# Kernel optimization log

Measured on AMD Instinct MI355X. Metric: run time of the kernel, lower is better.

## Reference

```python
import jax, jax.numpy as jnp
import numpy as np

N = 50000      # nodes
E = 800000     # edges
F_IN = 128     # in_channels
C = 64         # hidden_channels (per-head out channels)
H = 2          # heads
G = 256        # num graphs in batch
NEG_SLOPE = 0.2


def _gat_conv(x, src, dst, e_attr, W, att_src, att_dst, We, att_e, bias):
    """PyG GATConv with edge_dim, heads=H, concat=False, add_self_loops=True.
    x: [N, Fin]; src/dst: [Etot] (self-loops already appended); e_attr: [Etot, 1]."""
    n = x.shape[0]
    xp = (x @ W).reshape(n, H, C)                       # [N,H,C]
    ep = (e_attr @ We).reshape(-1, H, C)                # [Etot,H,C]
    a_src = jnp.einsum('nhc,hc->nh', xp, att_src)       # [N,H]
    a_dst = jnp.einsum('nhc,hc->nh', xp, att_dst)
    a_e = jnp.einsum('ehc,hc->eh', ep, att_e)
    alpha = a_src[src] + a_dst[dst] + a_e               # [Etot,H]
    alpha = jax.nn.leaky_relu(alpha, NEG_SLOPE)
    # softmax over edges grouped by destination node
    amax = jax.ops.segment_max(alpha, dst, num_segments=n)
    ex = jnp.exp(alpha - amax[dst])
    denom = jax.ops.segment_sum(ex, dst, num_segments=n)
    coef = ex / denom[dst]                              # [Etot,H]
    msg = coef[:, :, None] * xp[src]                    # [Etot,H,C]
    out = jax.ops.segment_sum(msg, dst, num_segments=n)  # [N,H,C]
    return out.mean(axis=1) + bias                      # concat=False -> head mean


def _add_self_loops(edge_index, edge_attr, n):
    loop = jnp.arange(n, dtype=edge_index.dtype)
    src = jnp.concatenate([edge_index[0], loop])
    dst = jnp.concatenate([edge_index[1], loop])
    fill = jnp.broadcast_to(edge_attr.mean(axis=0, keepdims=True), (n, edge_attr.shape[1]))
    ea = jnp.concatenate([edge_attr, fill], axis=0)
    return src, dst, ea


def setup_inputs() -> dict:
    key = jax.random.key(0)
    ks = jax.random.split(key, 20)
    s = 0.1
    inp = {
        'x': jax.random.normal(ks[0], (N, F_IN), jnp.float32),
        'edge_index': jax.random.randint(ks[1], (2, E), 0, N, jnp.int64),
        'edge_attr': jax.random.normal(ks[2], (E, 1), jnp.float32),
        'batch': jnp.sort(jax.random.randint(ks[3], (N,), 0, G, jnp.int64)),
        # GAT layer 1
        'W1': jax.random.normal(ks[4], (F_IN, H * C), jnp.float32) * s,
        'att_src1': jax.random.normal(ks[5], (H, C), jnp.float32) * s,
        'att_dst1': jax.random.normal(ks[6], (H, C), jnp.float32) * s,
        'We1': jax.random.normal(ks[7], (1, H * C), jnp.float32) * s,
        'att_e1': jax.random.normal(ks[8], (H, C), jnp.float32) * s,
        'b1': jnp.zeros((C,), jnp.float32),
        # GAT layer 2
        'W2': jax.random.normal(ks[9], (C, H * C), jnp.float32) * s,
        'att_src2': jax.random.normal(ks[10], (H, C), jnp.float32) * s,
        'att_dst2': jax.random.normal(ks[11], (H, C), jnp.float32) * s,
        'We2': jax.random.normal(ks[12], (1, H * C), jnp.float32) * s,
        'att_e2': jax.random.normal(ks[13], (H, C), jnp.float32) * s,
        'b2': jnp.zeros((C,), jnp.float32),
        # final linear
        'lin_w': jax.random.normal(ks[14], (C, 1), jnp.float32) * s,
        'lin_b': jnp.zeros((1,), jnp.float32),
    }
    return inp


def reference(x, edge_index, edge_attr, batch, W1, att_src1, att_dst1, We1, att_e1, b1,
              W2, att_src2, att_dst2, We2, att_e2, b2, lin_w, lin_b):
    src, dst, ea = _add_self_loops(edge_index, edge_attr, x.shape[0])
    h = jax.nn.relu(_gat_conv(x, src, dst, ea, W1, att_src1, att_dst1, We1, att_e1, b1))
    h = jax.nn.relu(_gat_conv(h, src, dst, ea, W2, att_src2, att_dst2, We2, att_e2, b2))
    # global mean pool over graphs
    sums = jax.ops.segment_sum(h, batch, num_segments=G)            # [G,C]
    cnts = jax.ops.segment_sum(jnp.ones((x.shape[0],), h.dtype), batch, num_segments=G)
    pooled = sums / jnp.maximum(cnts, 1.0)[:, None]
    return (pooled @ lin_w + lin_b).squeeze(-1)                      # [G]
```

## Files before the change

kernel.cpp:

```cpp
#include <hip/hip_runtime.h>


#define NEG_SLOPE 0.2f
#define CAP 64
#define RNG 128
#define AEDGE 4096
#define BCAP 40
typedef unsigned int uint;

__device__ __forceinline__ float wred_sum(float v) {
#pragma unroll
  for (int m = 32; m; m >>= 1) v += __shfl_xor(v, m);
  return v;
}
__device__ __forceinline__ float wred_max(float v) {
#pragma unroll
  for (int m = 32; m; m >>= 1) v = fmaxf(v, __shfl_xor(v, m));
  return v;
}
__device__ __forceinline__ float lrelu(float x) {
  return x > 0.0f ? x : NEG_SLOPE * x;
}
__device__ __forceinline__ uint bfpack(float a, float b) {
  uint ua = __float_as_uint(a), ub = __float_as_uint(b);
  ua = (ua + 0x7FFFu + ((ua >> 16) & 1u)) >> 16;
  ub = (ub + 0x7FFFu + ((ub >> 16) & 1u)) >> 16;
  return ua | (ub << 16);
}
__device__ __forceinline__ float4 bfunpack(uint2 v) {
  float4 f;
  f.x = __uint_as_float(v.x << 16);
  f.y = __uint_as_float(v.x & 0xFFFF0000u);
  f.z = __uint_as_float(v.y << 16);
  f.w = __uint_as_float(v.y & 0xFFFF0000u);
  return f;
}

#define BM 64
#define BK 32
__global__ __launch_bounds__(256) void fused_bin_gemm(
    const int* __restrict__ ei, const float* __restrict__ eattr, int E,
    int nbins, int ablks, int2* __restrict__ buck, int* __restrict__ cnt,
    float* __restrict__ partials,
    const float* __restrict__ X, const float* __restrict__ W,
    const float* __restrict__ att_src, const float* __restrict__ att_dst,
    uint* __restrict__ Y16, float* __restrict__ a_src,
    float* __restrict__ a_dst, int Nn, int K) {
  __shared__ float As[BK][68];
  __shared__ float Bs[BK][64];
  int t = threadIdx.x;

  if ((int)blockIdx.x < ablks) {
    int blk = blockIdx.x;
    int* cursor = (int*)As;
    float* red = ((float*)As) + 512;
    for (int i = t; i < nbins; i += 256) cursor[i] = 0;
    __syncthreads();
    int base = blk * AEDGE + t;
    float easum = 0.f;
#pragma unroll
    for (int k = 0; k < AEDGE / 256; ++k) {
      int i = base + k * 256;
      if (i < E) {
        int dv = ei[E + i];
        int sv = ei[i];
        float ev = eattr[i];
        easum += ev;
        int b = dv >> 7;
        int slot = atomicAdd(&cursor[b], 1);
        if (slot < BCAP) {
          int2 pl;
          pl.x = (sv << 7) | (dv & 127);
          pl.y = __float_as_int(ev);
          buck[((size_t)blk * nbins + b) * BCAP + slot] = pl;
        }
      }
    }
    __syncthreads();
    for (int b = t; b < nbins; b += 256)
      cnt[(size_t)b * ablks + blk] = min(cursor[b], BCAP);
    __syncthreads();
    red[t] = easum;
    __syncthreads();
    for (int off = 128; off; off >>= 1) {
      if (t < off) red[t] += red[t + off];
      __syncthreads();
    }
    if (t == 0) partials[blk] = red[0];
    return;
  }

  int g = (int)blockIdx.x - ablks;
  int tx = t & 15;
  int ty = t >> 4;
  int half = g & 1;
  int rowBase = (g >> 1) * BM;
  float acc[4][4];
#pragma unroll
  for (int r = 0; r < 4; ++r)
#pragma unroll
    for (int c = 0; c < 4; ++c) acc[r][c] = 0.f;

  for (int k0 = 0; k0 < K; k0 += BK) {
#pragma unroll
    for (int v = t; v < 512; v += 256) {
      int r = v >> 3;
      int cv = v & 7;
      int gr = rowBase + r;
      float4 a = make_float4(0.f, 0.f, 0.f, 0.f);
      if (gr < Nn) a = *(const float4*)(X + (size_t)gr * K + k0 + cv * 4);
      As[cv * 4 + 0][r] = a.x;
      As[cv * 4 + 1][r] = a.y;
      As[cv * 4 + 2][r] = a.z;
      As[cv * 4 + 3][r] = a.w;
    }
#pragma unroll
    for (int v = t; v < 512; v += 256) {
      int r = v >> 4;
      int cv = v & 15;
      *(float4*)&Bs[r][cv * 4] =
          *(const float4*)(W + (size_t)(k0 + r) * 128 + half * 64 + cv * 4);
    }
    __syncthreads();
#pragma unroll
    for (int kk = 0; kk < BK; ++kk) {
      float4 a = *(const float4*)&As[kk][ty * 4];
      float4 b = *(const float4*)&Bs[kk][tx * 4];
      acc[0][0] = fmaf(a.x, b.x, acc[0][0]);
      acc[0][1] = fmaf(a.x, b.y, acc[0][1]);
      acc[0][2] = fmaf(a.x, b.z, acc[0][2]);
      acc[0][3] = fmaf(a.x, b.w, acc[0][3]);
      acc[1][0] = fmaf(a.y, b.x, acc[1][0]);
      acc[1][1] = fmaf(a.y, b.y, acc[1][1]);
      acc[1][2] = fmaf(a.y, b.z, acc[1][2]);
      acc[1][3] = fmaf(a.y, b.w, acc[1][3]);
      acc[2][0] = fmaf(a.z, b.x, acc[2][0]);
      acc[2][1] = fmaf(a.z, b.y, acc[2][1]);
      acc[2][2] = fmaf(a.z, b.z, acc[2][2]);
      acc[2][3] = fmaf(a.z, b.w, acc[2][3]);
      acc[3][0] = fmaf(a.w, b.x, acc[3][0]);
      acc[3][1] = fmaf(a.w, b.y, acc[3][1]);
      acc[3][2] = fmaf(a.w, b.z, acc[3][2]);
      acc[3][3] = fmaf(a.w, b.w, acc[3][3]);
    }
    __syncthreads();
  }

  float attS[4], attD[4];
#pragma unroll
  for (int c = 0; c < 4; ++c) {
    attS[c] = att_src[half * 64 + tx * 4 + c];
    attD[c] = att_dst[half * 64 + tx * 4 + c];
  }
#pragma unroll
  for (int r = 0; r < 4; ++r) {
    int gr = rowBase + ty * 4 + r;
    float ps = 0.f, pd = 0.f;
#pragma unroll
    for (int c = 0; c < 4; ++c) {
      ps = fmaf(acc[r][c], attS[c], ps);
      pd = fmaf(acc[r][c], attD[c], pd);
    }
#pragma unroll
    for (int m = 1; m < 16; m <<= 1) {
      ps += __shfl_xor(ps, m);
      pd += __shfl_xor(pd, m);
    }
    if (gr < Nn) {
      if (tx == 0) {
        a_src[gr * 2 + half] = ps;
        a_dst[gr * 2 + half] = pd;
      }
      uint2 pk;
      pk.x = bfpack(acc[r][0], acc[r][1]);
      pk.y = bfpack(acc[r][2], acc[r][3]);
      *(uint2*)(Y16 + (size_t)gr * 64 + half * 32 + tx * 2) = pk;
    }
  }
}

__global__ __launch_bounds__(256) void passB(const int2* __restrict__ buck,
                                             const int* __restrict__ cnt,
                                             int nbins, int ablks, int N,
                                             int2* __restrict__ pay,
                                             int* __restrict__ fills) {
  __shared__ int pre[256];
  __shared__ int hist[128];
  int b = blockIdx.x;
  int t = threadIdx.x;
  if (t < 128) hist[t] = 0;
  int c = (t < ablks) ? cnt[(size_t)b * ablks + t] : 0;
  pre[t] = c;
  __syncthreads();
  for (int off = 1; off < 256; off <<= 1) {
    int v = (t >= off) ? pre[t - off] : 0;
    __syncthreads();
    pre[t] += v;
    __syncthreads();
  }
  int T = pre[255];
  int nodeBase = b << 7;
  for (int idx = t; idx < T; idx += 256) {
    int lo = 0, hi = 255;
    while (lo < hi) {
      int mid = (lo + hi) >> 1;
      if (pre[mid] > idx)
        hi = mid;
      else
        lo = mid + 1;
    }
    int blk = lo;
    int within = idx - (blk ? pre[blk - 1] : 0);
    int2 pl = buck[((size_t)blk * nbins + b) * BCAP + within];
    int dlo = pl.x & 127;
    int sv = pl.x >> 7;
    int slot = atomicAdd(&hist[dlo], 1);
    if (slot < CAP - 1) {
      int2 o;
      o.x = sv;
      o.y = pl.y;
      pay[((size_t)(nodeBase + dlo) << 6) + slot] = o;
    }
  }
  __syncthreads();
  if (t < 128) {
    int n = nodeBase + t;
    if (n < N) fills[n] = min(hist[t], CAP - 1);
  }
}

__global__ void finalize_params(const float* __restrict__ partials, int nparts,
                                int E, const float* __restrict__ We1,
                                const float* __restrict__ atte1,
                                const float* __restrict__ We2,
                                const float* __restrict__ atte2,
                                const float* __restrict__ W2,
                                const float* __restrict__ atts2,
                                const float* __restrict__ attd2,
                                float* __restrict__ params,
                                float* __restrict__ avec) {
  __shared__ float sm[256];
  int t = threadIdx.x;
  float s = 0.f;
  for (int i = t; i < nparts; i += 256) s += partials[i];
  sm[t] = s;
  __syncthreads();
  for (int off = 128; off; off >>= 1) {
    if (t < off) sm[t] += sm[t + off];
    __syncthreads();
  }
  if (t == 0) params[0] = sm[0] / (float)E;
  __syncthreads();
  int l = t >> 7, h = (t >> 6) & 1, c = t & 63;
  float p = (l == 0) ? We1[h * 64 + c] * atte1[h * 64 + c]
                     : We2[h * 64 + c] * atte2[h * 64 + c];
  sm[t] = p;
  __syncthreads();
  for (int off = 32; off; off >>= 1) {
    if (c < off) sm[t] += sm[t + off];
    __syncthreads();
  }
  if (c == 0) params[1 + l * 2 + h] = sm[t];
  int k = t & 63;
  const float* att = (l == 0) ? atts2 : attd2;
  float acc = 0.f;
#pragma unroll 4
  for (int cc = 0; cc < 64; ++cc)
    acc = fmaf(W2[k * 128 + h * 64 + cc], att[h * 64 + cc], acc);
  avec[l * 128 + h * 64 + k] = acc;
}

__global__ __launch_bounds__(256, 8) void gat_gather_l1(
    const int* __restrict__ fills, const int2* __restrict__ pay,
    const uint* __restrict__ xp16, const float* __restrict__ a_src1,
    const float* __restrict__ a_dst, const float* __restrict__ params,
    const float* __restrict__ bias, const float* __restrict__ avec,
    uint* __restrict__ h16, float* __restrict__ a_src2,
    float* __restrict__ a_dst2, int N) {
  __shared__ float sm_c[4][128];
  __shared__ uint sm_s[4][64];
  int wid = threadIdx.x >> 6, lane = threadIdx.x & 63;
  int n = blockIdx.x * 4 + wid;
  if (n >= N) return;
  int beg = n << 6;
  int dg = min(fills[n], CAP - 1) + 1;
  float s0 = params[1], s1 = params[2];
  float ad0 = a_dst[n * 2 + 0], ad1 = a_dst[n * 2 + 1];
  const uint2* xp2 = (const uint2*)xp16;

  float al0 = -1e30f, al1 = -1e30f;
  uint myS = (uint)n * 32u;
  if (lane < dg) {
    int sidx = n;
    float eav = params[0];
    if (lane != dg - 1) {
      int2 pe = pay[beg + lane];
      sidx = pe.x;
      eav = __int_as_float(pe.y);
      myS = (uint)pe.x * 32u;
    }
    float2 as = *(const float2*)(a_src1 + (size_t)sidx * 2);
    al0 = lrelu(as.x + ad0 + eav * s0);
    al1 = lrelu(as.y + ad1 + eav * s1);
  }
  float m0 = wred_max(al0), m1 = wred_max(al1);
  float e0 = __expf(al0 - m0), e1 = __expf(al1 - m1);
  float sum0 = wred_sum(e0), sum1 = wred_sum(e1);
  sm_c[wid][lane * 2 + 0] = e0 / sum0;
  sm_c[wid][lane * 2 + 1] = e1 / sum1;
  sm_s[wid][lane] = myS;

  int half = lane >> 5;
  uint l5 = lane & 31;
  int h = (lane >> 4) & 1;
  const float* sc = sm_c[wid];
  const uint* ss = sm_s[wid];
  float4 acc = make_float4(0.f, 0.f, 0.f, 0.f);

  for (int e0i = 0; e0i < dg; e0i += 8) {
    int ea = e0i + half;
    int eb = e0i + 2 + half;
    int ec = e0i + 4 + half;
    int ed = e0i + 6 + half;
    uint2 ua = xp2[ss[ea] + l5];
    uint2 ub = xp2[ss[eb] + l5];
    uint2 uc = xp2[ss[ec] + l5];
    uint2 ud = xp2[ss[ed] + l5];
    float ca = sc[ea * 2 + h], cb = sc[eb * 2 + h];
    float cc2 = sc[ec * 2 + h], cd = sc[ed * 2 + h];
    float4 va = bfunpack(ua);
    float4 vb = bfunpack(ub);
    float4 vc = bfunpack(uc);
    float4 vd = bfunpack(ud);
    acc.x = fmaf(ca, va.x, acc.x);
    acc.y = fmaf(ca, va.y, acc.y);
    acc.z = fmaf(ca, va.z, acc.z);
    acc.w = fmaf(ca, va.w, acc.w);
    acc.x = fmaf(cb, vb.x, acc.x);
    acc.y = fmaf(cb, vb.y, acc.y);
    acc.z = fmaf(cb, vb.z, acc.z);
    acc.w = fmaf(cb, vb.w, acc.w);
    acc.x = fmaf(cc2, vc.x, acc.x);
    acc.y = fmaf(cc2, vc.y, acc.y);
    acc.z = fmaf(cc2, vc.z, acc.z);
    acc.w = fmaf(cc2, vc.w, acc.w);
    acc.x = fmaf(cd, vd.x, acc.x);
    acc.y = fmaf(cd, vd.y, acc.y);
    acc.z = fmaf(cd, vd.z, acc.z);
    acc.w = fmaf(cd, vd.w, acc.w);
  }

  acc.x += __shfl_xor(acc.x, 32);
  acc.y += __shfl_xor(acc.y, 32);
  acc.z += __shfl_xor(acc.z, 32);
  acc.w += __shfl_xor(acc.w, 32);
  float4 oth;
  oth.x = __shfl_xor(acc.x, 16);
  oth.y = __shfl_xor(acc.y, 16);
  oth.z = __shfl_xor(acc.z, 16);
  oth.w = __shfl_xor(acc.w, 16);

  float ps0 = 0.f, ps1 = 0.f, pd0 = 0.f, pd1 = 0.f;
  if (lane < 16) {
    float4 b = *(const float4*)(bias + lane * 4);
    float4 o;
    o.x = fmaxf(0.5f * (acc.x + oth.x) + b.x, 0.f);
    o.y = fmaxf(0.5f * (acc.y + oth.y) + b.y, 0.f);
    o.z = fmaxf(0.5f * (acc.z + oth.z) + b.z, 0.f);
    o.w = fmaxf(0.5f * (acc.w + oth.w) + b.w, 0.f);
    uint2 hp;
    hp.x = bfpack(o.x, o.y);
    hp.y = bfpack(o.z, o.w);
    *(uint2*)(h16 + (size_t)n * 32 + lane * 2) = hp;
    float4 vs0 = *(const float4*)(avec + lane * 4);
    float4 vs1 = *(const float4*)(avec + 64 + lane * 4);
    float4 vd0 = *(const float4*)(avec + 128 + lane * 4);
    float4 vd1 = *(const float4*)(avec + 192 + lane * 4);
    ps0 = o.x * vs0.x + o.y * vs0.y + o.z * vs0.z + o.w * vs0.w;
    ps1 = o.x * vs1.x + o.y * vs1.y + o.z * vs1.z + o.w * vs1.w;
    pd0 = o.x * vd0.x + o.y * vd0.y + o.z * vd0.z + o.w * vd0.w;
    pd1 = o.x * vd1.x + o.y * vd1.y + o.z * vd1.z + o.w * vd1.w;
  }
#pragma unroll
  for (int m = 1; m < 16; m <<= 1) {
    ps0 += __shfl_xor(ps0, m);
    ps1 += __shfl_xor(ps1, m);
    pd0 += __shfl_xor(pd0, m);
    pd1 += __shfl_xor(pd1, m);
  }
  if (lane == 0) {
    a_src2[n * 2 + 0] = ps0;
    a_src2[n * 2 + 1] = ps1;
    a_dst2[n * 2 + 0] = pd0;
    a_dst2[n * 2 + 1] = pd1;
  }
}

__global__ __launch_bounds__(256, 8) void gat_gather_l2(
    const int* __restrict__ fills, const int2* __restrict__ pay,
    const uint* __restrict__ h16, const float* __restrict__ a_src,
    const float* __restrict__ a_dst, const float* __restrict__ params,
    float* __restrict__ agg, int N) {
  __shared__ float sm_c[4][128];
  __shared__ uint sm_s[4][64];
  int wid = threadIdx.x >> 6, lane = threadIdx.x & 63;
  int n = blockIdx.x * 4 + wid;
  if (n >= N) return;
  int beg = n << 6;
  int dg = min(fills[n], CAP - 1) + 1;
  float s0 = params[3], s1 = params[4];
  float ad0 = a_dst[n * 2 + 0], ad1 = a_dst[n * 2 + 1];
  const uint2* h2 = (const uint2*)h16;

  float al0 = -1e30f, al1 = -1e30f;
  uint myOff = (uint)n * 16u;
  if (lane < dg) {
    int sidx = n;
    float eav = params[0];
    if (lane != dg - 1) {
      int2 pe = pay[beg + lane];
      sidx = pe.x;
      eav = __int_as_float(pe.y);
      myOff = (uint)pe.x * 16u;
    }
    float2 as = *(const float2*)(a_src + (size_t)sidx * 2);
    al0 = lrelu(as.x + ad0 + eav * s0);
    al1 = lrelu(as.y + ad1 + eav * s1);
  }
  float m0 = wred_max(al0), m1 = wred_max(al1);
  float e0 = __expf(al0 - m0), e1 = __expf(al1 - m1);
  float sum0 = wred_sum(e0), sum1 = wred_sum(e1);
  sm_c[wid][lane * 2 + 0] = e0 / sum0;
  sm_c[wid][lane * 2 + 1] = e1 / sum1;
  sm_s[wid][lane] = myOff;

  int q = lane >> 4;
  uint l4 = lane & 15;
  const float* sc = sm_c[wid];
  const uint* ss = sm_s[wid];
  float4 a0 = make_float4(0.f, 0.f, 0.f, 0.f);
  float4 a1 = make_float4(0.f, 0.f, 0.f, 0.f);

  for (int e0i = 0; e0i < dg; e0i += 16) {
    int ea = e0i + q;
    int eb = e0i + 4 + q;
    int ec = e0i + 8 + q;
    int ed = e0i + 12 + q;
    uint2 ua = h2[ss[ea] + l4];
    uint2 ub = h2[ss[eb] + l4];
    uint2 uc = h2[ss[ec] + l4];
    uint2 ud = h2[ss[ed] + l4];
    float c0a = sc[ea * 2], c1a = sc[ea * 2 + 1];
    float c0b = sc[eb * 2], c1b = sc[eb * 2 + 1];
    float c0c = sc[ec * 2], c1c = sc[ec * 2 + 1];
    float c0d = sc[ed * 2], c1d = sc[ed * 2 + 1];
    float4 va = bfunpack(ua);
    float4 vb = bfunpack(ub);
    float4 vc = bfunpack(uc);
    float4 vd = bfunpack(ud);
    a0.x = fmaf(c0a, va.x, a0.x);
    a0.y = fmaf(c0a, va.y, a0.y);
    a0.z = fmaf(c0a, va.z, a0.z);
    a0.w = fmaf(c0a, va.w, a0.w);
    a1.x = fmaf(c1a, va.x, a1.x);
    a1.y = fmaf(c1a, va.y, a1.y);
    a1.z = fmaf(c1a, va.z, a1.z);
    a1.w = fmaf(c1a, va.w, a1.w);
    a0.x = fmaf(c0b, vb.x, a0.x);
    a0.y = fmaf(c0b, vb.y, a0.y);
    a0.z = fmaf(c0b, vb.z, a0.z);
    a0.w = fmaf(c0b, vb.w, a0.w);
    a1.x = fmaf(c1b, vb.x, a1.x);
    a1.y = fmaf(c1b, vb.y, a1.y);
    a1.z = fmaf(c1b, vb.z, a1.z);
    a1.w = fmaf(c1b, vb.w, a1.w);
    a0.x = fmaf(c0c, vc.x, a0.x);
    a0.y = fmaf(c0c, vc.y, a0.y);
    a0.z = fmaf(c0c, vc.z, a0.z);
    a0.w = fmaf(c0c, vc.w, a0.w);
    a1.x = fmaf(c1c, vc.x, a1.x);
    a1.y = fmaf(c1c, vc.y, a1.y);
    a1.z = fmaf(c1c, vc.z, a1.z);
    a1.w = fmaf(c1c, vc.w, a1.w);
    a0.x = fmaf(c0d, vd.x, a0.x);
    a0.y = fmaf(c0d, vd.y, a0.y);
    a0.z = fmaf(c0d, vd.z, a0.z);
    a0.w = fmaf(c0d, vd.w, a0.w);
    a1.x = fmaf(c1d, vd.x, a1.x);
    a1.y = fmaf(c1d, vd.y, a1.y);
    a1.z = fmaf(c1d, vd.z, a1.z);
    a1.w = fmaf(c1d, vd.w, a1.w);
  }

#pragma unroll
  for (int m = 16; m <= 32; m <<= 1) {
    a0.x += __shfl_xor(a0.x, m);
    a0.y += __shfl_xor(a0.y, m);
    a0.z += __shfl_xor(a0.z, m);
    a0.w += __shfl_xor(a0.w, m);
    a1.x += __shfl_xor(a1.x, m);
    a1.y += __shfl_xor(a1.y, m);
    a1.z += __shfl_xor(a1.z, m);
    a1.w += __shfl_xor(a1.w, m);
  }
  if (lane < 16) {
    *(float4*)(agg + (size_t)n * 128 + lane * 4) = a0;
    *(float4*)(agg + (size_t)n * 128 + 64 + lane * 4) = a1;
  }
}

__global__ __launch_bounds__(256) void gemm_final(
    const float* __restrict__ agg, const float* __restrict__ W2,
    const float* __restrict__ b2, const float* __restrict__ lin_w,
    float* __restrict__ dotv, int N) {
  __shared__ float As[BK][68];
  __shared__ float Bs[BK][64];
  int t = threadIdx.x;
  int tx = t & 15;
  int ty = t >> 4;
  int rowBase = blockIdx.x * BM;
  float acc[4][4];
#pragma unroll
  for (int r = 0; r < 4; ++r)
#pragma unroll
    for (int c = 0; c < 4; ++c) acc[r][c] = 0.f;

  for (int k0 = 0; k0 < 128; k0 += BK) {
#pragma unroll
    for (int v = t; v < 512; v += 256) {
      int r = v >> 3;
      int cv = v & 7;
      int gr = rowBase + r;
      float4 a = make_float4(0.f, 0.f, 0.f, 0.f);
      if (gr < N) a = *(const float4*)(agg + (size_t)gr * 128 + k0 + cv * 4);
      As[cv * 4 + 0][r] = a.x;
      As[cv * 4 + 1][r] = a.y;
      As[cv * 4 + 2][r] = a.z;
      As[cv * 4 + 3][r] = a.w;
    }
#pragma unroll
    for (int v = t; v < BK * 64 / 4; v += 256) {
      int r = v >> 4;
      int cv = v & 15;
      int k = k0 + r;
      const float* src = (k < 64) ? W2 + (size_t)k * 128 + cv * 4
                                  : W2 + (size_t)(k - 64) * 128 + 64 + cv * 4;
      *(float4*)&Bs[r][cv * 4] = *(const float4*)src;
    }
    __syncthreads();
#pragma unroll
    for (int kk = 0; kk < BK; ++kk) {
      float4 a = *(const float4*)&As[kk][ty * 4];
      float4 b = *(const float4*)&Bs[kk][tx * 4];
      acc[0][0] = fmaf(a.x, b.x, acc[0][0]);
      acc[0][1] = fmaf(a.x, b.y, acc[0][1]);
      acc[0][2] = fmaf(a.x, b.z, acc[0][2]);
      acc[0][3] = fmaf(a.x, b.w, acc[0][3]);
      acc[1][0] = fmaf(a.y, b.x, acc[1][0]);
      acc[1][1] = fmaf(a.y, b.y, acc[1][1]);
      acc[1][2] = fmaf(a.y, b.z, acc[1][2]);
      acc[1][3] = fmaf(a.y, b.w, acc[1][3]);
      acc[2][0] = fmaf(a.z, b.x, acc[2][0]);
      acc[2][1] = fmaf(a.z, b.y, acc[2][1]);
      acc[2][2] = fmaf(a.z, b.z, acc[2][2]);
      acc[2][3] = fmaf(a.z, b.w, acc[2][3]);
      acc[3][0] = fmaf(a.w, b.x, acc[3][0]);
      acc[3][1] = fmaf(a.w, b.y, acc[3][1]);
      acc[3][2] = fmaf(a.w, b.z, acc[3][2]);
      acc[3][3] = fmaf(a.w, b.w, acc[3][3]);
    }
    __syncthreads();
  }

  float bb[4], lw[4];
#pragma unroll
  for (int c = 0; c < 4; ++c) {
    bb[c] = b2[tx * 4 + c];
    lw[c] = lin_w[tx * 4 + c];
  }
#pragma unroll
  for (int r = 0; r < 4; ++r) {
    int gr = rowBase + ty * 4 + r;
    float p = 0.f;
#pragma unroll
    for (int c = 0; c < 4; ++c) {
      float val = fmaxf(0.5f * acc[r][c] + bb[c], 0.f);
      p = fmaf(val, lw[c], p);
    }
#pragma unroll
    for (int m = 1; m < 16; m <<= 1) p += __shfl_xor(p, m);
    if (gr < N && tx == 0) dotv[gr] = p;
  }
}

__device__ __forceinline__ int lowerb(const int* b, int n, int v) {
  int lo = 0, hi = n;
  while (lo < hi) {
    int mid = (lo + hi) >> 1;
    if (b[mid] < v)
      lo = mid + 1;
    else
      hi = mid;
  }
  return lo;
}

__global__ void pool_lin(const float* __restrict__ dot,
                         const int* __restrict__ batch, int N, int G,
                         const float* __restrict__ lin_b,
                         float* __restrict__ out) {
  int g = blockIdx.x;
  int lane = threadIdx.x;
  int beg = lowerb(batch, N, g);
  int end = lowerb(batch, N, g + 1);
  float s = 0.f;
  for (int i = beg + lane; i < end; i += 64) s += dot[i];
  s = wred_sum(s);
  if (lane == 0) {
    float cnt = fmaxf((float)(end - beg), 1.0f);
    out[g] = s / cnt + lin_b[0];
  }
}

extern "C" void kernel_launch(void* const* d_in, const int* in_sizes, int n_in,
                              void* d_out, int out_size, void* d_ws,
                              size_t ws_size, hipStream_t stream) {
  const float* x = (const float*)d_in[0];
  const int* ei = (const int*)d_in[1];
  const float* eattr = (const float*)d_in[2];
  const int* batch = (const int*)d_in[3];
  const float* W1 = (const float*)d_in[4];
  const float* att_src1 = (const float*)d_in[5];
  const float* att_dst1 = (const float*)d_in[6];
  const float* We1 = (const float*)d_in[7];
  const float* att_e1 = (const float*)d_in[8];
  const float* b1 = (const float*)d_in[9];
  const float* W2 = (const float*)d_in[10];
  const float* att_src2 = (const float*)d_in[11];
  const float* att_dst2 = (const float*)d_in[12];
  const float* We2 = (const float*)d_in[13];
  const float* att_e2 = (const float*)d_in[14];
  const float* b2 = (const float*)d_in[15];
  const float* lin_w = (const float*)d_in[16];
  const float* lin_b = (const float*)d_in[17];
  float* out = (float*)d_out;

  const int Nn = in_sizes[0] / 128;
  const int Ee = in_sizes[2];
  const int Gg = out_size;

  char* ws = (char*)d_ws;
  size_t off = 0;
  auto alloc = [&](size_t bytes) -> char* {
    char* p = ws + off;
    off += (bytes + 255) & ~(size_t)255;
    return p;
  };

  const int nbins = (Nn + RNG - 1) / RNG;
  const int ablks = (Ee + AEDGE - 1) / AEDGE;
  const int gemmBlocks = ((Nn + BM - 1) / BM) * 2;

  float* params = (float*)alloc(8 * 4);
  float* avec = (float*)alloc(256 * 4);
  float* partials = (float*)alloc((size_t)(ablks + 8) * 4);
  int* fills = (int*)alloc((size_t)Nn * 4);
  int2* pay = (int2*)alloc((size_t)Nn * CAP * 8);
  int2* buck = (int2*)alloc((size_t)ablks * nbins * BCAP * 8);
  int* cnt = (int*)alloc((size_t)nbins * ablks * 4);
  float* a_src = (float*)alloc((size_t)Nn * 2 * 4);
  float* a_dst = (float*)alloc((size_t)Nn * 2 * 4);
  float* a_src2 = (float*)alloc((size_t)Nn * 2 * 4);
  float* a_dst2 = (float*)alloc((size_t)Nn * 2 * 4);
  float* agg = (float*)alloc((size_t)Nn * 128 * 4);
  uint* xp16 = (uint*)alloc((size_t)Nn * 64 * 4);
  uint* h16 = (uint*)alloc((size_t)Nn * 32 * 4);
  float* dotv = (float*)alloc((size_t)Nn * 4);

  fused_bin_gemm<<<ablks + gemmBlocks, 256, 0, stream>>>(
      ei, eattr, Ee, nbins, ablks, buck, cnt, partials, x, W1, att_src1,
      att_dst1, xp16, a_src, a_dst, Nn, 128);
  passB<<<nbins, 256, 0, stream>>>(buck, cnt, nbins, ablks, Nn, pay, fills);
  finalize_params<<<1, 256, 0, stream>>>(partials, ablks, Ee, We1, att_e1,
                                         We2, att_e2, W2, att_src2, att_dst2,
                                         params, avec);

  gat_gather_l1<<<(Nn + 3) / 4, 256, 0, stream>>>(fills, pay, xp16, a_src,
                                                  a_dst, params, b1, avec, h16,
                                                  a_src2, a_dst2, Nn);
  gat_gather_l2<<<(Nn + 3) / 4, 256, 0, stream>>>(fills, pay, h16, a_src2,
                                                  a_dst2, params, agg, Nn);
  gemm_final<<<(Nn + BM - 1) / BM, 256, 0, stream>>>(agg, W2, b2, lin_w, dotv,
                                                     Nn);
  pool_lin<<<Gg, 64, 0, stream>>>(dotv, batch, Nn, Gg, lin_b, out);
}
```

Baseline: 149.1 us.

## Fold param finalize into passB and widen gather loads to 16-byte vectors

The separate single-block finalize_params kernel is removed, and its work now runs as an extra block of passB, saving one kernel launch. Both GAT gather kernels now load bf16 feature rows with uint4 (16-byte) instead of uint2 loads. Each lane therefore covers 8 channels, and more edges are handled per wave-slice, which needs an extra shuffle-reduction step. This cuts the number of memory instructions in the gather but doubles the accumulator registers per lane.

Result: slower. 160.4 us (+7.6%).

```diff
diff --git a/kernel.cpp b/kernel.cpp
--- a/kernel.cpp
+++ b/kernel.cpp
@@ -27,12 +27,12 @@
   ub = (ub + 0x7FFFu + ((ub >> 16) & 1u)) >> 16;
   return ua | (ub << 16);
 }
-__device__ __forceinline__ float4 bfunpack(uint2 v) {
+__device__ __forceinline__ float4 bfunpack2(uint a, uint b) {
   float4 f;
-  f.x = __uint_as_float(v.x << 16);
-  f.y = __uint_as_float(v.x & 0xFFFF0000u);
-  f.z = __uint_as_float(v.y << 16);
-  f.w = __uint_as_float(v.y & 0xFFFF0000u);
+  f.x = __uint_as_float(a << 16);
+  f.y = __uint_as_float(a & 0xFFFF0000u);
+  f.z = __uint_as_float(b << 16);
+  f.w = __uint_as_float(b & 0xFFFF0000u);
   return f;
 }
 
@@ -41,11 +41,10 @@
 __global__ __launch_bounds__(256) void fused_bin_gemm(
     const int* __restrict__ ei, const float* __restrict__ eattr, int E,
     int nbins, int ablks, int2* __restrict__ buck, int* __restrict__ cnt,
-    float* __restrict__ partials,
-    const float* __restrict__ X, const float* __restrict__ W,
-    const float* __restrict__ att_src, const float* __restrict__ att_dst,
-    uint* __restrict__ Y16, float* __restrict__ a_src,
-    float* __restrict__ a_dst, int Nn, int K) {
+    float* __restrict__ partials, const float* __restrict__ X,
+    const float* __restrict__ W, const float* __restrict__ att_src,
+    const float* __restrict__ att_dst, uint* __restrict__ Y16,
+    float* __restrict__ a_src, float* __restrict__ a_dst, int Nn, int K) {
   __shared__ float As[BK][68];
   __shared__ float Bs[BK][64];
   int t = threadIdx.x;
@@ -179,15 +178,51 @@
   }
 }
 
-__global__ __launch_bounds__(256) void passB(const int2* __restrict__ buck,
-                                             const int* __restrict__ cnt,
-                                             int nbins, int ablks, int N,
-                                             int2* __restrict__ pay,
-                                             int* __restrict__ fills) {
+__global__ __launch_bounds__(256) void passB(
+    const int2* __restrict__ buck, const int* __restrict__ cnt, int nbins,
+    int ablks, int N, int2* __restrict__ pay, int* __restrict__ fills,
+    const float* __restrict__ partials, int E, const float* __restrict__ We1,
+    const float* __restrict__ atte1, const float* __restrict__ We2,
+    const float* __restrict__ atte2, const float* __restrict__ W2,
+    const float* __restrict__ atts2, const float* __restrict__ attd2,
+    float* __restrict__ params, float* __restrict__ avec) {
   __shared__ int pre[256];
   __shared__ int hist[128];
   int b = blockIdx.x;
   int t = threadIdx.x;
+
+  if (b == nbins) {
+    float* sm = (float*)pre;
+    float s = 0.f;
+    for (int i = t; i < ablks; i += 256) s += partials[i];
+    sm[t] = s;
+    __syncthreads();
+    for (int off = 128; off; off >>= 1) {
+      if (t < off) sm[t] += sm[t + off];
+      __syncthreads();
+    }
+    if (t == 0) params[0] = sm[0] / (float)E;
+    __syncthreads();
+    int l = t >> 7, h = (t >> 6) & 1, c = t & 63;
+    float p = (l == 0) ? We1[h * 64 + c] * atte1[h * 64 + c]
+                       : We2[h * 64 + c] * atte2[h * 64 + c];
+    sm[t] = p;
+    __syncthreads();
+    for (int off = 32; off; off >>= 1) {
+      if (c < off) sm[t] += sm[t + off];
+      __syncthreads();
+    }
+    if (c == 0) params[1 + l * 2 + h] = sm[t];
+    int k = t & 63;
+    const float* att = (l == 0) ? atts2 : attd2;
+    float acc = 0.f;
+#pragma unroll 4
+    for (int cc = 0; cc < 64; ++cc)
+      acc = fmaf(W2[k * 128 + h * 64 + cc], att[h * 64 + cc], acc);
+    avec[l * 128 + h * 64 + k] = acc;
+    return;
+  }
+
   if (t < 128) hist[t] = 0;
   int c = (t < ablks) ? cnt[(size_t)b * ablks + t] : 0;
   pre[t] = c;
@@ -227,47 +262,6 @@
     int n = nodeBase + t;
     if (n < N) fills[n] = min(hist[t], CAP - 1);
   }
-}
-
-__global__ void finalize_params(const float* __restrict__ partials, int nparts,
-                                int E, const float* __restrict__ We1,
-                                const float* __restrict__ atte1,
-                                const float* __restrict__ We2,
-                                const float* __restrict__ atte2,
-                                const float* __restrict__ W2,
-                                const float* __restrict__ atts2,
-                                const float* __restrict__ attd2,
-                                float* __restrict__ params,
-                                float* __restrict__ avec) {
-  __shared__ float sm[256];
-  int t = threadIdx.x;
-  float s = 0.f;
-  for (int i = t; i < nparts; i += 256) s += partials[i];
-  sm[t] = s;
-  __syncthreads();
-  for (int off = 128; off; off >>= 1) {
-    if (t < off) sm[t] += sm[t + off];
-    __syncthreads();
-  }
-  if (t == 0) params[0] = sm[0] / (float)E;
-  __syncthreads();
-  int l = t >> 7, h = (t >> 6) & 1, c = t & 63;
-  float p = (l == 0) ? We1[h * 64 + c] * atte1[h * 64 + c]
-                     : We2[h * 64 + c] * atte2[h * 64 + c];
-  sm[t] = p;
-  __syncthreads();
-  for (int off = 32; off; off >>= 1) {
-    if (c < off) sm[t] += sm[t + off];
-    __syncthreads();
-  }
-  if (c == 0) params[1 + l * 2 + h] = sm[t];
-  int k = t & 63;
-  const float* att = (l == 0) ? atts2 : attd2;
-  float acc = 0.f;
-#pragma unroll 4
-  for (int cc = 0; cc < 64; ++cc)
-    acc = fmaf(W2[k * 128 + h * 64 + cc], att[h * 64 + cc], acc);
-  avec[l * 128 + h * 64 + k] = acc;
 }
 
 __global__ __launch_bounds__(256, 8) void gat_gather_l1(
@@ -286,10 +280,10 @@
   int dg = min(fills[n], CAP - 1) + 1;
   float s0 = params[1], s1 = params[2];
   float ad0 = a_dst[n * 2 + 0], ad1 = a_dst[n * 2 + 1];
-  const uint2* xp2 = (const uint2*)xp16;
+  const uint4* xp4 = (const uint4*)xp16;
 
   float al0 = -1e30f, al1 = -1e30f;
-  uint myS = (uint)n * 32u;
+  uint myS = (uint)n * 16u;
   if (lane < dg) {
     int sidx = n;
     float eav = params[0];
@@ -297,7 +291,7 @@
       int2 pe = pay[beg + lane];
       sidx = pe.x;
       eav = __int_as_float(pe.y);
-      myS = (uint)pe.x * 32u;
+      myS = (uint)pe.x * 16u;
     }
     float2 as = *(const float2*)(a_src1 + (size_t)sidx * 2);
     al0 = lrelu(as.x + ad0 + eav * s0);
@@ -310,79 +304,102 @@
   sm_c[wid][lane * 2 + 1] = e1 / sum1;
   sm_s[wid][lane] = myS;
 
-  int half = lane >> 5;
-  uint l5 = lane & 31;
-  int h = (lane >> 4) & 1;
+  int q = lane >> 4;
+  uint l4 = lane & 15u;
+  int h = (int)(l4 >> 3);
   const float* sc = sm_c[wid];
   const uint* ss = sm_s[wid];
-  float4 acc = make_float4(0.f, 0.f, 0.f, 0.f);
+  float4 aL = make_float4(0.f, 0.f, 0.f, 0.f);
+  float4 aH = make_float4(0.f, 0.f, 0.f, 0.f);
 
   for (int e0i = 0; e0i < dg; e0i += 8) {
-    int ea = e0i + half;
-    int eb = e0i + 2 + half;
-    int ec = e0i + 4 + half;
-    int ed = e0i + 6 + half;
-    uint2 ua = xp2[ss[ea] + l5];
-    uint2 ub = xp2[ss[eb] + l5];
-    uint2 uc = xp2[ss[ec] + l5];
-    uint2 ud = xp2[ss[ed] + l5];
+    int ea = e0i + q;
+    int eb = e0i + 4 + q;
+    uint4 ua = xp4[ss[ea] + l4];
+    uint4 ub = xp4[ss[eb] + l4];
     float ca = sc[ea * 2 + h], cb = sc[eb * 2 + h];
-    float cc2 = sc[ec * 2 + h], cd = sc[ed * 2 + h];
-    float4 va = bfunpack(ua);
-    float4 vb = bfunpack(ub);
-    float4 vc = bfunpack(uc);
-    float4 vd = bfunpack(ud);
-    acc.x = fmaf(ca, va.x, acc.x);
-    acc.y = fmaf(ca, va.y, acc.y);
-    acc.z = fmaf(ca, va.z, acc.z);
-    acc.w = fmaf(ca, va.w, acc.w);
-    acc.x = fmaf(cb, vb.x, acc.x);
-    acc.y = fmaf(cb, vb.y, acc.y);
-    acc.z = fmaf(cb, vb.z, acc.z);
-    acc.w = fmaf(cb, vb.w, acc.w);
-    acc.x = fmaf(cc2, vc.x, acc.x);
-    acc.y = fmaf(cc2, vc.y, acc.y);
-    acc.z = fmaf(cc2, vc.z, acc.z);
-    acc.w = fmaf(cc2, vc.w, acc.w);
-    acc.x = fmaf(cd, vd.x, acc.x);
-    acc.y = fmaf(cd, vd.y, acc.y);
-    acc.z = fmaf(cd, vd.z, acc.z);
-    acc.w = fmaf(cd, vd.w, acc.w);
-  }
-
-  acc.x += __shfl_xor(acc.x, 32);
-  acc.y += __shfl_xor(acc.y, 32);
-  acc.z += __shfl_xor(acc.z, 32);
-  acc.w += __shfl_xor(acc.w, 32);
-  float4 oth;
-  oth.x = __shfl_xor(acc.x, 16);
-  oth.y = __shfl_xor(acc.y, 16);
-  oth.z = __shfl_xor(acc.z, 16);
-  oth.w = __shfl_xor(acc.w, 16);
+    float4 va0 = bfunpack2(ua.x, ua.y);
+    float4 va1 = bfunpack2(ua.z, ua.w);
+    float4 vb0 = bfunpack2(ub.x, ub.y);
+    float4 vb1 = bfunpack2(ub.z, ub.w);
+    aL.x = fmaf(ca, va0.x, aL.x);
+    aL.y = fmaf(ca, va0.y, aL.y);
+    aL.z = fmaf(ca, va0.z, aL.z);
+    aL.w = fmaf(ca, va0.w, aL.w);
+    aH.x = fmaf(ca, va1.x, aH.x);
+    aH.y = fmaf(ca, va1.y, aH.y);
+    aH.z = fmaf(ca, va1.z, aH.z);
+    aH.w = fmaf(ca, va1.w, aH.w);
+    aL.x = fmaf(cb, vb0.x, aL.x);
+    aL.y = fmaf(cb, vb0.y, aL.y);
+    aL.z = fmaf(cb, vb0.z, aL.z);
+    aL.w = fmaf(cb, vb0.w, aL.w);
+    aH.x = fmaf(cb, vb1.x, aH.x);
+    aH.y = fmaf(cb, vb1.y, aH.y);
+    aH.z = fmaf(cb, vb1.z, aH.z);
+    aH.w = fmaf(cb, vb1.w, aH.w);
+  }
+
+#pragma unroll
+  for (int m = 16; m <= 32; m <<= 1) {
+    aL.x += __shfl_xor(aL.x, m);
+    aL.y += __shfl_xor(aL.y, m);
+    aL.z += __shfl_xor(aL.z, m);
+    aL.w += __shfl_xor(aL.w, m);
+    aH.x += __shfl_xor(aH.x, m);
+    aH.y += __shfl_xor(aH.y, m);
+    aH.z += __shfl_xor(aH.z, m);
+    aH.w += __shfl_xor(aH.w, m);
+  }
+  float4 oL, oH;
+  oL.x = __shfl_xor(aL.x, 8);
+  oL.y = __shfl_xor(aL.y, 8);
+  oL.z = __shfl_xor(aL.z, 8);
+  oL.w = __shfl_xor(aL.w, 8);
+  oH.x = __shfl_xor(aH.x, 8);
+  oH.y = __shfl_xor(aH.y, 8);
+  oH.z = __shfl_xor(aH.z, 8);
+  oH.w = __shfl_xor(aH.w, 8);
 
   float ps0 = 0.f, ps1 = 0.f, pd0 = 0.f, pd1 = 0.f;
-  if (lane < 16) {
-    float4 b = *(const float4*)(bias + lane * 4);
-    float4 o;
-    o.x = fmaxf(0.5f * (acc.x + oth.x) + b.x, 0.f);
-    o.y = fmaxf(0.5f * (acc.y + oth.y) + b.y, 0.f);
-    o.z = fmaxf(0.5f * (acc.z + oth.z) + b.z, 0.f);
-    o.w = fmaxf(0.5f * (acc.w + oth.w) + b.w, 0.f);
-    uint2 hp;
-    hp.x = bfpack(o.x, o.y);
-    hp.y = bfpack(o.z, o.w);
-    *(uint2*)(h16 + (size_t)n * 32 + lane * 2) = hp;
-    float4 vs0 = *(const float4*)(avec + lane * 4);
-    float4 vs1 = *(const float4*)(avec + 64 + lane * 4);
-    float4 vd0 = *(const float4*)(avec + 128 + lane * 4);
-    float4 vd1 = *(const float4*)(avec + 192 + lane * 4);
-    ps0 = o.x * vs0.x + o.y * vs0.y + o.z * vs0.z + o.w * vs0.w;
-    ps1 = o.x * vs1.x + o.y * vs1.y + o.z * vs1.z + o.w * vs1.w;
-    pd0 = o.x * vd0.x + o.y * vd0.y + o.z * vd0.z + o.w * vd0.w;
-    pd1 = o.x * vd1.x + o.y * vd1.y + o.z * vd1.z + o.w * vd1.w;
-  }
-#pragma unroll
-  for (int m = 1; m < 16; m <<= 1) {
+  if (lane < 8) {
+    float4 b0 = *(const float4*)(bias + lane * 8);
+    float4 b1 = *(const float4*)(bias + lane * 8 + 4);
+    float4 o0, o1;
+    o0.x = fmaxf(0.5f * (aL.x + oL.x) + b0.x, 0.f);
+    o0.y = fmaxf(0.5f * (aL.y + oL.y) + b0.y, 0.f);
+    o0.z = fmaxf(0.5f * (aL.z + oL.z) + b0.z, 0.f);
+    o0.w = fmaxf(0.5f * (aL.w + oL.w) + b0.w, 0.f);
+    o1.x = fmaxf(0.5f * (aH.x + oH.x) + b1.x, 0.f);
+    o1.y = fmaxf(0.5f * (aH.y + oH.y) + b1.y, 0.f);
+    o1.z = fmaxf(0.5f * (aH.z + oH.z) + b1.z, 0.f);
+    o1.w = fmaxf(0.5f * (aH.w + oH.w) + b1.w, 0.f);
+    uint4 hp;
+    hp.x = bfpack(o0.x, o0.y);
+    hp.y = bfpack(o0.z, o0.w);
+    hp.z = bfpack(o1.x, o1.y);
+    hp.w = bfpack(o1.z, o1.w);
+    *(uint4*)(h16 + (size_t)n * 32 + lane * 4) = hp;
+    float4 u, v;
+    u = *(const float4*)(avec + lane * 8);
+    v = *(const float4*)(avec + lane * 8 + 4);
+    ps0 = o0.x * u.x + o0.y * u.y + o0.z * u.z + o0.w * u.w + o1.x * v.x +
+          o1.y * v.y + o1.z * v.z + o1.w * v.w;
+    u = *(const float4*)(avec + 64 + lane * 8);
+    v = *(const float4*)(avec + 64 + lane * 8 + 4);
+    ps1 = o0.x * u.x + o0.y * u.y + o0.z * u.z + o0.w * u.w + o1.x * v.x +
+          o1.y * v.y + o1.z * v.z + o1.w * v.w;
+    u = *(const float4*)(avec + 128 + lane * 8);
+    v = *(const float4*)(avec + 128 + lane * 8 + 4);
+    pd0 = o0.x * u.x + o0.y * u.y + o0.z * u.z + o0.w * u.w + o1.x * v.x +
+          o1.y * v.y + o1.z * v.z + o1.w * v.w;
+    u = *(const float4*)(avec + 192 + lane * 8);
+    v = *(const float4*)(avec + 192 + lane * 8 + 4);
+    pd1 = o0.x * u.x + o0.y * u.y + o0.z * u.z + o0.w * u.w + o1.x * v.x +
+          o1.y * v.y + o1.z * v.z + o1.w * v.w;
+  }
+#pragma unroll
+  for (int m = 1; m < 8; m <<= 1) {
     ps0 += __shfl_xor(ps0, m);
     ps1 += __shfl_xor(ps1, m);
     pd0 += __shfl_xor(pd0, m);
@@ -410,10 +427,10 @@
   int dg = min(fills[n], CAP - 1) + 1;
   float s0 = params[3], s1 = params[4];
   float ad0 = a_dst[n * 2 + 0], ad1 = a_dst[n * 2 + 1];
-  const uint2* h2 = (const uint2*)h16;
+  const uint4* h4 = (const uint4*)h16;
 
   float al0 = -1e30f, al1 = -1e30f;
-  uint myOff = (uint)n * 16u;
+  uint myOff = (uint)n * 8u;
   if (lane < dg) {
     int sidx = n;
     float eav = params[0];
@@ -421,7 +438,7 @@
       int2 pe = pay[beg + lane];
       sidx = pe.x;
       eav = __int_as_float(pe.y);
-      myOff = (uint)pe.x * 16u;
+      myOff = (uint)pe.x * 8u;
     }
     float2 as = *(const float2*)(a_src + (size_t)sidx * 2);
     al0 = lrelu(as.x + ad0 + eav * s0);
@@ -434,78 +451,85 @@
   sm_c[wid][lane * 2 + 1] = e1 / sum1;
   sm_s[wid][lane] = myOff;
 
-  int q = lane >> 4;
-  uint l4 = lane & 15;
+  int oct = lane >> 3;
+  uint l3 = lane & 7u;
   const float* sc = sm_c[wid];
   const uint* ss = sm_s[wid];
-  float4 a0 = make_float4(0.f, 0.f, 0.f, 0.f);
-  float4 a1 = make_float4(0.f, 0.f, 0.f, 0.f);
+  float4 a0L = make_float4(0.f, 0.f, 0.f, 0.f);
+  float4 a0H = make_float4(0.f, 0.f, 0.f, 0.f);
+  float4 a1L = make_float4(0.f, 0.f, 0.f, 0.f);
+  float4 a1H = make_float4(0.f, 0.f, 0.f, 0.f);
 
   for (int e0i = 0; e0i < dg; e0i += 16) {
-    int ea = e0i + q;
-    int eb = e0i + 4 + q;
-    int ec = e0i + 8 + q;
-    int ed = e0i + 12 + q;
-    uint2 ua = h2[ss[ea] + l4];
-    uint2 ub = h2[ss[eb] + l4];
-    uint2 uc = h2[ss[ec] + l4];
-    uint2 ud = h2[ss[ed] + l4];
+    int ea = e0i + oct;
+    int eb = e0i + 8 + oct;
+    uint4 ua = h4[ss[ea] + l3];
+    uint4 ub = h4[ss[eb] + l3];
     float c0a = sc[ea * 2], c1a = sc[ea * 2 + 1];
     float c0b = sc[eb * 2], c1b = sc[eb * 2 + 1];
-    float c0c = sc[ec * 2], c1c = sc[ec * 2 + 1];
-    float c0d = sc[ed * 2], c1d = sc[ed * 2 + 1];
-    float4 va = bfunpack(ua);
-    float4 vb = bfunpack(ub);
-    float4 vc = bfunpack(uc);
-    float4 vd = bfunpack(ud);
-    a0.x = fmaf(c0a, va.x, a0.x);
-    a0.y = fmaf(c0a, va.y, a0.y);
-    a0.z = fmaf(c0a, va.z, a0.z);
-    a0.w = fmaf(c0a, va.w, a0.w);
-    a1.x = fmaf(c1a, va.x, a1.x);
-    a1.y = fmaf(c1a, va.y, a1.y);
-    a1.z = fmaf(c1a, va.z, a1.z);
-    a1.w = fmaf(c1a, va.w, a1.w);
-    a0.x = fmaf(c0b, vb.x, a0.x);
-    a0.y = fmaf(c0b, vb.y, a0.y);
-    a0.z = fmaf(c0b, vb.z, a0.z);
-    a0.w = fmaf(c0b, vb.w, a0.w);
-    a1.x = fmaf(c1b, vb.x, a1.x);
-    a1.y = fmaf(c1b, vb.y, a1.y);
-    a1.z = fmaf(c1b, vb.z, a1.z);
-    a1.w = fmaf(c1b, vb.w, a1.w);
-    a0.x = fmaf(c0c, vc.x, a0.x);
-    a0.y = fmaf(c0c, vc.y, a0.y);
-    a0.z = fmaf(c0c, vc.z, a0.z);
-    a0.w = fmaf(c0c, vc.w, a0.w);
-    a1.x = fmaf(c1c, vc.x, a1.x);
-    a1.y = fmaf(c1c, vc.y, a1.y);
-    a1.z = fmaf(c1c, vc.z, a1.z);
-    a1.w = fmaf(c1c, vc.w, a1.w);
-    a0.x = fmaf(c0d, vd.x, a0.x);
-    a0.y = fmaf(c0d, vd.y, a0.y);
-    a0.z = fmaf(c0d, vd.z, a0.z);
-    a0.w = fmaf(c0d, vd.w, a0.w);
-    a1.x = fmaf(c1d, vd.x, a1.x);
-    a1.y = fmaf(c1d, vd.y, a1.y);
-    a1.z = fmaf(c1d, vd.z, a1.z);
-    a1.w = fmaf(c1d, vd.w, a1.w);
-  }
-
-#pragma unroll
-  for (int m = 16; m <= 32; m <<= 1) {
-    a0.x += __shfl_xor(a0.x, m);
-    a0.y += __shfl_xor(a0.y, m);
-    a0.z += __shfl_xor(a0.z, m);
-    a0.w += __shfl_xor(a0.w, m);
-    a1.x += __shfl_xor(a1.x, m);
-    a1.y += __shfl_xor(a1.y, m);
-    a1.z += __shfl_xor(a1.z, m);
-    a1.w += __shfl_xor(a1.w, m);
-  }
-  if (lane < 16) {
-    *(float4*)(agg + (size_t)n * 128 + lane * 4) = a0;
-    *(float4*)(agg + (size_t)n * 128 + 64 + lane * 4) = a1;
+    float4 vA0 = bfunpack2(ua.x, ua.y);
+    float4 vA1 = bfunpack2(ua.z, ua.w);
+    float4 vB0 = bfunpack2(ub.x, ub.y);
+    float4 vB1 = bfunpack2(ub.z, ub.w);
+    a0L.x = fmaf(c0a, vA0.x, a0L.x);
+    a0L.y = fmaf(c0a, vA0.y, a0L.y);
+    a0L.z = fmaf(c0a, vA0.z, a0L.z);
+    a0L.w = fmaf(c0a, vA0.w, a0L.w);
+    a0H.x = fmaf(c0a, vA1.x, a0H.x);
+    a0H.y = fmaf(c0a, vA1.y, a0H.y);
+    a0H.z = fmaf(c0a, vA1.z, a0H.z);
+    a0H.w = fmaf(c0a, vA1.w, a0H.w);
+    a1L.x = fmaf(c1a, vA0.x, a1L.x);
+    a1L.y = fmaf(c1a, vA0.y, a1L.y);
+    a1L.z = fmaf(c1a, vA0.z, a1L.z);
+    a1L.w = fmaf(c1a, vA0.w, a1L.w);
+    a1H.x = fmaf(c1a, vA1.x, a1H.x);
+    a1H.y = fmaf(c1a, vA1.y, a1H.y);
+    a1H.z = fmaf(c1a, vA1.z, a1H.z);
+    a1H.w = fmaf(c1a, vA1.w, a1H.w);
+    a0L.x = fmaf(c0b, vB0.x, a0L.x);
+    a0L.y = fmaf(c0b, vB0.y, a0L.y);
+    a0L.z = fmaf(c0b, vB0.z, a0L.z);
+    a0L.w = fmaf(c0b, vB0.w, a0L.w);
+    a0H.x = fmaf(c0b, vB1.x, a0H.x);
+    a0H.y = fmaf(c0b, vB1.y, a0H.y);
+    a0H.z = fmaf(c0b, vB1.z, a0H.z);
+    a0H.w = fmaf(c0b, vB1.w, a0H.w);
+    a1L.x = fmaf(c1b, vB0.x, a1L.x);
+    a1L.y = fmaf(c1b, vB0.y, a1L.y);
+    a1L.z = fmaf(c1b, vB0.z, a1L.z);
+    a1L.w = fmaf(c1b, vB0.w, a1L.w);
+    a1H.x = fmaf(c1b, vB1.x, a1H.x);
+    a1H.y = fmaf(c1b, vB1.y, a1H.y);
+    a1H.z = fmaf(c1b, vB1.z, a1H.z);
+    a1H.w = fmaf(c1b, vB1.w, a1H.w);
+  }
+
+#pragma unroll
+  for (int m = 8; m <= 32; m <<= 1) {
+    a0L.x += __shfl_xor(a0L.x, m);
+    a0L.y += __shfl_xor(a0L.y, m);
+    a0L.z += __shfl_xor(a0L.z, m);
+    a0L.w += __shfl_xor(a0L.w, m);
+    a0H.x += __shfl_xor(a0H.x, m);
+    a0H.y += __shfl_xor(a0H.y, m);
+    a0H.z += __shfl_xor(a0H.z, m);
+    a0H.w += __shfl_xor(a0H.w, m);
+    a1L.x += __shfl_xor(a1L.x, m);
+    a1L.y += __shfl_xor(a1L.y, m);
+    a1L.z += __shfl_xor(a1L.z, m);
+    a1L.w += __shfl_xor(a1L.w, m);
+    a1H.x += __shfl_xor(a1H.x, m);
+    a1H.y += __shfl_xor(a1H.y, m);
+    a1H.z += __shfl_xor(a1H.z, m);
+    a1H.w += __shfl_xor(a1H.w, m);
+  }
+  if (lane < 8) {
+    float* dst = agg + (size_t)n * 128 + lane * 8;
+    *(float4*)(dst) = a0L;
+    *(float4*)(dst + 4) = a0H;
+    *(float4*)(dst + 64) = a1L;
+    *(float4*)(dst + 68) = a1H;
   }
 }
 
@@ -680,10 +704,9 @@
   fused_bin_gemm<<<ablks + gemmBlocks, 256, 0, stream>>>(
       ei, eattr, Ee, nbins, ablks, buck, cnt, partials, x, W1, att_src1,
       att_dst1, xp16, a_src, a_dst, Nn, 128);
-  passB<<<nbins, 256, 0, stream>>>(buck, cnt, nbins, ablks, Nn, pay, fills);
-  finalize_params<<<1, 256, 0, stream>>>(partials, ablks, Ee, We1, att_e1,
-                                         We2, att_e2, W2, att_src2, att_dst2,
-                                         params, avec);
+  passB<<<nbins + 1, 256, 0, stream>>>(buck, cnt, nbins, ablks, Nn, pay, fills,
+                                       partials, Ee, We1, att_e1, We2, att_e2,
+                                       W2, att_src2, att_dst2, params, avec);
 
   gat_gather_l1<<<(Nn + 3) / 4, 256, 0, stream>>>(fills, pay, xp16, a_src,
                                                   a_dst, params, b1, avec, h16,
```
